# Performance work log

Hardware: AMD Instinct MI355X
Metric: run time of the kernel (lower is better)

## Reference

```python
import jax, jax.numpy as jnp
import numpy as np

NUM_EMBEDDINGS = 8192
EMBEDDING_DIM = 512
COMMITMENT_COST = 0.25
DECAY = 0.99
EPSILON = 1e-05


def _l2_normalize(x, axis=-1, eps=1e-12):
    # matches torch.nn.functional.normalize (p=2)
    n = jnp.sqrt(jnp.sum(x * x, axis=axis, keepdims=True))
    return x / jnp.maximum(n, eps)


def setup_inputs() -> dict:
    key = jax.random.key(0)
    k1, k2, k3 = jax.random.split(key, 3)
    inputs = jax.random.normal(k1, (8, 4096, EMBEDDING_DIM), dtype=jnp.float32)
    embedding = jax.random.normal(k2, (NUM_EMBEDDINGS, EMBEDDING_DIM), dtype=jnp.float32) * 0.01
    ema_cluster_size = jnp.ones((NUM_EMBEDDINGS,), dtype=jnp.float32)
    ema_w = jax.random.normal(k3, (NUM_EMBEDDINGS, EMBEDDING_DIM), dtype=jnp.float32) * 0.01
    return {"inputs": inputs, "embedding": embedding,
            "ema_cluster_size": ema_cluster_size, "ema_w": ema_w}


def reference(inputs, embedding, ema_cluster_size, ema_w):
    K, D = NUM_EMBEDDINGS, EMBEDDING_DIM
    flat = _l2_normalize(inputs.reshape(-1, D))           # [N, D]
    emb_n = _l2_normalize(embedding)                       # [K, D] (in-place normalize in torch)

    # cosine distance: 1 - flat @ emb^T  -> argmin
    distances = 1.0 - jnp.matmul(flat, emb_n.T)            # [N, K]
    idx = jnp.argmin(distances, axis=1)                    # [N]

    # one-hot @ codebook == gather
    quantized = jnp.take(emb_n, idx, axis=0).reshape(inputs.shape)

    # EMA codebook update (training branch), scatter-encode via segment_sum
    counts = jax.ops.segment_sum(jnp.ones_like(idx, dtype=flat.dtype), idx,
                                 num_segments=K)           # [K]
    new_cs = ema_cluster_size * DECAY + (1.0 - DECAY) * counts
    n = jnp.sum(new_cs)
    new_cs = (new_cs + EPSILON) / (n + K * EPSILON) * n
    dw = jax.ops.segment_sum(flat, idx, num_segments=K)    # [K, D] == one_hot^T @ flat
    new_ema_w = ema_w * DECAY + (1.0 - DECAY) * dw
    new_embedding = new_ema_w / jnp.clip(new_cs, EPSILON, None)[:, None]

    e_latent_loss = jnp.mean((jax.lax.stop_gradient(quantized) - inputs) ** 2)
    loss = COMMITMENT_COST * e_latent_loss

    quantized_st = inputs + jax.lax.stop_gradient(quantized - inputs)
    encoding_indices = idx.reshape(inputs.shape[:-1])
    return (quantized_st, loss, encoding_indices, new_cs, new_ema_w, new_embedding)
```

## Files before the change

### kernel.cpp

```cpp
#include <hip/hip_runtime.h>
#include <math.h>

#define NROWS 32768
#define DIM   512
#define KCODE 8192
#define DECAYF 0.99f
#define OMDF   0.01f
#define EPSF   1e-5f
#define COMMITF 0.25f
#define MARGIN 8e-4f

typedef _Float16 half8 __attribute__((ext_vector_type(8)));
typedef _Float16 half4v __attribute__((ext_vector_type(4)));
typedef _Float16 half2v __attribute__((ext_vector_type(2)));
typedef float floatx16 __attribute__((ext_vector_type(16)));


__device__ __forceinline__ float block_sum_256(float v) {
    __shared__ float sm[4];
    int lane = threadIdx.x & 63, wave = threadIdx.x >> 6;
    #pragma unroll
    for (int off = 32; off; off >>= 1) v += __shfl_down(v, off);
    if (lane == 0) sm[wave] = v;
    __syncthreads();
    if (threadIdx.x == 0) v = sm[0] + sm[1] + sm[2] + sm[3];
    return v;
}

__global__ void k_rownorm_inv(const float* __restrict__ x, float* __restrict__ inv) {
    int wave = threadIdx.x >> 6;
    int lane = threadIdx.x & 63;
    int row = blockIdx.x * 4 + wave;
    const float* p = x + (size_t)row * DIM;
    float4 f1 = *(const float4*)&p[lane * 4];
    float4 f2 = *(const float4*)&p[256 + lane * 4];
    float s = f1.x*f1.x + f1.y*f1.y + f1.z*f1.z + f1.w*f1.w
            + f2.x*f2.x + f2.y*f2.y + f2.z*f2.z + f2.w*f2.w;
    #pragma unroll
    for (int off = 32; off; off >>= 1) s += __shfl_down(s, off);
    if (lane == 0) inv[row] = 1.0f / fmaxf(sqrtf(s), 1e-12f);
}

__global__ void k_split(const float* __restrict__ src, const float* __restrict__ inv,
                        _Float16* __restrict__ hi, _Float16* __restrict__ lo) {
    const int i4 = (blockIdx.x * 256 + threadIdx.x) * 4;
    const float iv = inv[i4 >> 9];
    const float4 v = *(const float4*)&src[i4];
    float n0 = v.x * iv, n1 = v.y * iv, n2 = v.z * iv, n3 = v.w * iv;
    _Float16 h0 = (_Float16)n0, h1 = (_Float16)n1, h2 = (_Float16)n2, h3 = (_Float16)n3;
    half4v hv = {h0, h1, h2, h3};
    *(half4v*)&hi[i4] = hv;
    half4v lv = {(_Float16)((n0 - (float)h0) * 4096.f),
                 (_Float16)((n1 - (float)h1) * 4096.f),
                 (_Float16)((n2 - (float)h2) * 4096.f),
                 (_Float16)((n3 - (float)h3) * 4096.f)};
    *(half4v*)&lo[i4] = lv;
}

__device__ __forceinline__ void gld16(const _Float16* g, _Float16* l) {
    __builtin_amdgcn_global_load_lds(
        (const __attribute__((address_space(1))) void*)g,
        (__attribute__((address_space(3))) void*)l, 16, 0, 0);
}

__device__ __forceinline__ void top2_upd(float v, int i, float& v1, int& i1, float& v2) {
    if (v > v1) { v2 = v1; v1 = v; i1 = i; }
    else        { v2 = fmaxf(v2, v); }
}

__launch_bounds__(256, 2)
__global__ void k_hi(const _Float16* __restrict__ Xh, const _Float16* __restrict__ Eh,
                     float* __restrict__ sV1, float* __restrict__ sV2,
                     unsigned short* __restrict__ sI1) {
    __shared__ __align__(16) _Float16 lds[24576];
    __shared__ float mV[128][2], mV2[128][2];
    __shared__ int   mI[128][2];

    const int tid  = threadIdx.x;
    const int w    = tid >> 6;
    const int lane = tid & 63;
    const int wc = w & 1, wr = w >> 1;
    const int c = lane & 31, h = lane >> 5;
    const int rowBase = blockIdx.x * 128;
    const int split   = blockIdx.y;
    const int sr = lane >> 3;
    const int sg = (lane & 7) ^ (sr & 7);
    const int cx = c & 7;
    const int rowB = wr * 64 + c;

    float v1a = -1e30f, v2a = -1e30f, v1b = -1e30f, v2b = -1e30f;
    int i1a = 0, i1b = 0;

    for (int nt = 0; nt < 16; ++nt) {
        const int ntBase = split * 4096 + nt * 256;
        floatx16 acc[4][2];
        #pragma unroll
        for (int i = 0; i < 4; ++i)
            #pragma unroll
            for (int j = 0; j < 2; ++j)
                #pragma unroll
                for (int r = 0; r < 16; ++r) acc[i][j][r] = 0.f;

        for (int chunk = 0; chunk < 8; ++chunk) {
            const int kt = chunk * 64;
            #pragma unroll
            for (int j = 0; j < 12; ++j) {
                const int u0 = w * 96 + j * 8;
                const int u  = u0 + sr;
                if (u0 < 256) {
                    gld16(Eh + (size_t)(ntBase + u) * DIM + kt + sg * 8, &lds[u0 * 64]);
                } else {
                    gld16(Xh + (size_t)(rowBase + u - 256) * DIM + kt + sg * 8,
                          &lds[16384 + (u0 - 256) * 64]);
                }
            }
            __syncthreads();
            #pragma unroll
            for (int ks = 0; ks < 4; ++ks) {
                const int so = ((ks * 2 + h) ^ cx) * 8;
                half8 a0 = *(const half8*)&lds[(wc * 128 + 0  + c) * 64 + so];
                half8 a1 = *(const half8*)&lds[(wc * 128 + 32 + c) * 64 + so];
                half8 a2 = *(const half8*)&lds[(wc * 128 + 64 + c) * 64 + so];
                half8 a3 = *(const half8*)&lds[(wc * 128 + 96 + c) * 64 + so];
                half8 b0 = *(const half8*)&lds[16384 + (rowB) * 64 + so];
                half8 b1 = *(const half8*)&lds[16384 + (rowB + 32) * 64 + so];
                acc[0][0] = __builtin_amdgcn_mfma_f32_32x32x16_f16(a0, b0, acc[0][0], 0, 0, 0);
                acc[1][0] = __builtin_amdgcn_mfma_f32_32x32x16_f16(a1, b0, acc[1][0], 0, 0, 0);
                acc[2][0] = __builtin_amdgcn_mfma_f32_32x32x16_f16(a2, b0, acc[2][0], 0, 0, 0);
                acc[3][0] = __builtin_amdgcn_mfma_f32_32x32x16_f16(a3, b0, acc[3][0], 0, 0, 0);
                acc[0][1] = __builtin_amdgcn_mfma_f32_32x32x16_f16(a0, b1, acc[0][1], 0, 0, 0);
                acc[1][1] = __builtin_amdgcn_mfma_f32_32x32x16_f16(a1, b1, acc[1][1], 0, 0, 0);
                acc[2][1] = __builtin_amdgcn_mfma_f32_32x32x16_f16(a2, b1, acc[2][1], 0, 0, 0);
                acc[3][1] = __builtin_amdgcn_mfma_f32_32x32x16_f16(a3, b1, acc[3][1], 0, 0, 0);
            }
            __syncthreads();
        }
        #pragma unroll
        for (int r = 0; r < 16; ++r) {
            const int codeSub = (r & 3) + ((r >> 2) << 3) + (h << 2);
            #pragma unroll
            for (int i = 0; i < 4; ++i) {
                const int code = ntBase + wc * 128 + i * 32 + codeSub;
                top2_upd(acc[i][0][r], code, v1a, i1a, v2a);
                top2_upd(acc[i][1][r], code, v1b, i1b, v2b);
            }
        }
    }

    {
        float ov1 = __shfl_xor(v1a, 32); int oi1 = __shfl_xor(i1a, 32); float ov2 = __shfl_xor(v2a, 32);
        if (ov1 > v1a) { v2a = fmaxf(v1a, ov2); v1a = ov1; i1a = oi1; }
        else if (ov1 == v1a) { v2a = v1a; if (oi1 < i1a) i1a = oi1; }
        else { v2a = fmaxf(v2a, ov1); }
        ov1 = __shfl_xor(v1b, 32); oi1 = __shfl_xor(i1b, 32); ov2 = __shfl_xor(v2b, 32);
        if (ov1 > v1b) { v2b = fmaxf(v1b, ov2); v1b = ov1; i1b = oi1; }
        else if (ov1 == v1b) { v2b = v1b; if (oi1 < i1b) i1b = oi1; }
        else { v2b = fmaxf(v2b, ov1); }
    }
    if (h == 0) {
        mV[rowB][wc] = v1a; mV2[rowB][wc] = v2a; mI[rowB][wc] = i1a;
        mV[rowB + 32][wc] = v1b; mV2[rowB + 32][wc] = v2b; mI[rowB + 32][wc] = i1b;
    }
    __syncthreads();
    if (tid < 128) {
        float v1 = mV[tid][0], v2 = mV2[tid][0]; int i1 = mI[tid][0];
        float ov1 = mV[tid][1], ov2 = mV2[tid][1]; int oi1 = mI[tid][1];
        if (ov1 > v1) { v2 = fmaxf(v1, ov2); v1 = ov1; i1 = oi1; }
        else if (ov1 == v1) { v2 = v1; if (oi1 < i1) i1 = oi1; }
        else { v2 = fmaxf(v2, ov1); }
        const int n = rowBase + tid;
        sV1[split * NROWS + n] = v1;
        sV2[split * NROWS + n] = v2;
        sI1[split * NROWS + n] = (unsigned short)i1;
    }
}

__global__ void k_top2_merge(const float* __restrict__ sV1, const float* __restrict__ sV2,
                             const unsigned short* __restrict__ sI1,
                             float* __restrict__ outIdx, int* __restrict__ list,
                             int* __restrict__ flagCnt) {
    const int n = blockIdx.x * 256 + threadIdx.x;
    float a1 = sV1[n], a2 = sV2[n]; int ai = sI1[n];
    float b1 = sV1[NROWS + n], b2 = sV2[NROWS + n]; int bi = sI1[NROWS + n];
    float best, run; int bidx;
    if (b1 > a1) { best = b1; bidx = bi; run = fmaxf(a1, b2); }
    else         { best = a1; bidx = ai; run = fmaxf(a2, b1); }
    outIdx[n] = (float)bidx;
    if (best - run < MARGIN) {
        int p = atomicAdd(flagCnt, 1);
        list[p] = n;
    }
}

__device__ __forceinline__ unsigned long long encodeKey(float v, int idx) {
    unsigned u = __float_as_uint(v);
    u = (u & 0x80000000u) ? ~u : (u | 0x80000000u);
    return ((unsigned long long)u << 32) | (unsigned)(0xFFFFFFFFu - (unsigned)idx);
}

__launch_bounds__(256, 2)
__global__ void k_rescore(const _Float16* __restrict__ Xh, const _Float16* __restrict__ Xl,
                          const _Float16* __restrict__ Eh, const _Float16* __restrict__ El,
                          const int* __restrict__ list, const int* __restrict__ flagCnt,
                          unsigned long long* __restrict__ rkey) {
    const int cnt = *flagCnt;
    const int t = blockIdx.x & 255;
    const int s = blockIdx.x >> 8;
    if (t * 128 >= cnt) return;

    __shared__ __align__(16) _Float16 lds[32768];
    __shared__ float mV[128][2];
    __shared__ int   mI[128][2];

    const int tid  = threadIdx.x;
    const int w    = tid >> 6;
    const int lane = tid & 63;
    const int wc = w & 1, wr = w >> 1;
    const int c = lane & 31, h = lane >> 5;
    const int sr = lane >> 3;
    const int sg = (lane & 7) ^ (sr & 7);
    const int rowA = wc * 64 + c;
    const int rowB = wr * 64 + c;
    const int cx = c & 7;

    int rows_j[4];
    #pragma unroll
    for (int j = 0; j < 4; ++j) {
        const int slot = t * 128 + w * 32 + j * 8 + sr;
        rows_j[j] = (slot < cnt) ? list[slot] : 0;
    }

    float best0 = -1e30f, best1 = -1e30f;
    int bi0 = 0, bi1 = 0;
    const float SC = 1.0f / 4096.0f;

    for (int nt = 0; nt < 4; ++nt) {
        const int ntBase = s * 512 + nt * 128;

        floatx16 accH00, accH01, accH10, accH11, accC00, accC01, accC10, accC11;
        #pragma unroll
        for (int r = 0; r < 16; ++r) {
            accH00[r] = 0.f; accH01[r] = 0.f; accH10[r] = 0.f; accH11[r] = 0.f;
            accC00[r] = 0.f; accC01[r] = 0.f; accC10[r] = 0.f; accC11[r] = 0.f;
        }

        for (int chunk = 0; chunk < 8; ++chunk) {
            const int kt = chunk * 64;
            #pragma unroll
            for (int j = 0; j < 4; ++j) {
                const int rl = w * 32 + j * 8 + sr;
                const size_t gE = (size_t)(ntBase + rl) * DIM + kt + sg * 8;
                const size_t gX = (size_t)rows_j[j] * DIM + kt + sg * 8;
                _Float16* dBase = &lds[(w * 32 + j * 8) * 64];
                gld16(Eh + gE, dBase);
                gld16(El + gE, dBase + 8192);
                gld16(Xh + gX, dBase + 16384);
                gld16(Xl + gX, dBase + 24576);
            }
            __syncthreads();
            #pragma unroll
            for (int ks = 0; ks < 4; ++ks) {
                const int so = ((ks * 2 + h) ^ cx) * 8;
                const half8 ah0 = *(const half8*)&lds[rowA * 64 + so];
                const half8 ah1 = *(const half8*)&lds[(rowA + 32) * 64 + so];
                const half8 al0 = *(const half8*)&lds[8192 + rowA * 64 + so];
                const half8 al1 = *(const half8*)&lds[8192 + (rowA + 32) * 64 + so];
                const half8 bh0 = *(const half8*)&lds[16384 + rowB * 64 + so];
                const half8 bh1 = *(const half8*)&lds[16384 + (rowB + 32) * 64 + so];
                const half8 bl0 = *(const half8*)&lds[24576 + rowB * 64 + so];
                const half8 bl1 = *(const half8*)&lds[24576 + (rowB + 32) * 64 + so];

                accH00 = __builtin_amdgcn_mfma_f32_32x32x16_f16(ah0, bh0, accH00, 0, 0, 0);
                accC00 = __builtin_amdgcn_mfma_f32_32x32x16_f16(ah0, bl0, accC00, 0, 0, 0);
                accC00 = __builtin_amdgcn_mfma_f32_32x32x16_f16(al0, bh0, accC00, 0, 0, 0);

                accH01 = __builtin_amdgcn_mfma_f32_32x32x16_f16(ah0, bh1, accH01, 0, 0, 0);
                accC01 = __builtin_amdgcn_mfma_f32_32x32x16_f16(ah0, bl1, accC01, 0, 0, 0);
                accC01 = __builtin_amdgcn_mfma_f32_32x32x16_f16(al0, bh1, accC01, 0, 0, 0);

                accH10 = __builtin_amdgcn_mfma_f32_32x32x16_f16(ah1, bh0, accH10, 0, 0, 0);
                accC10 = __builtin_amdgcn_mfma_f32_32x32x16_f16(ah1, bl0, accC10, 0, 0, 0);
                accC10 = __builtin_amdgcn_mfma_f32_32x32x16_f16(al1, bh0, accC10, 0, 0, 0);

                accH11 = __builtin_amdgcn_mfma_f32_32x32x16_f16(ah1, bh1, accH11, 0, 0, 0);
                accC11 = __builtin_amdgcn_mfma_f32_32x32x16_f16(ah1, bl1, accC11, 0, 0, 0);
                accC11 = __builtin_amdgcn_mfma_f32_32x32x16_f16(al1, bh1, accC11, 0, 0, 0);
            }
            __syncthreads();
        }

        #pragma unroll
        for (int r = 0; r < 16; ++r) {
            const int codeSub = (r & 3) + ((r >> 2) << 3) + (h << 2);
            const int code0 = ntBase + wc * 64 + codeSub;
            const int code1 = code0 + 32;
            float v;
            v = fmaf(accC00[r], SC, accH00[r]);
            if (v > best0 || (v == best0 && code0 < bi0)) { best0 = v; bi0 = code0; }
            v = fmaf(accC10[r], SC, accH10[r]);
            if (v > best0 || (v == best0 && code1 < bi0)) { best0 = v; bi0 = code1; }
            v = fmaf(accC01[r], SC, accH01[r]);
            if (v > best1 || (v == best1 && code0 < bi1)) { best1 = v; bi1 = code0; }
            v = fmaf(accC11[r], SC, accH11[r]);
            if (v > best1 || (v == best1 && code1 < bi1)) { best1 = v; bi1 = code1; }
        }
    }

    {
        float ov = __shfl_xor(best0, 32); int oi = __shfl_xor(bi0, 32);
        if (ov > best0 || (ov == best0 && oi < bi0)) { best0 = ov; bi0 = oi; }
        ov = __shfl_xor(best1, 32); oi = __shfl_xor(bi1, 32);
        if (ov > best1 || (ov == best1 && oi < bi1)) { best1 = ov; bi1 = oi; }
    }
    if (h == 0) {
        mV[rowB][wc] = best0;      mI[rowB][wc] = bi0;
        mV[rowB + 32][wc] = best1; mI[rowB + 32][wc] = bi1;
    }
    __syncthreads();
    if (tid < 128) {
        const int slot = t * 128 + tid;
        if (slot < cnt) {
            float v0 = mV[tid][0]; int i0 = mI[tid][0];
            float v1 = mV[tid][1]; int i1 = mI[tid][1];
            float bv; int bidx;
            if (v1 > v0 || (v1 == v0 && i1 < i0)) { bv = v1; bidx = i1; }
            else                                  { bv = v0; bidx = i0; }
            atomicMax(&rkey[list[slot]], encodeKey(bv, bidx));
        }
    }
}

__global__ void k_rescore_merge(const unsigned long long* __restrict__ rkey,
                                const int* __restrict__ list, const int* __restrict__ flagCnt,
                                float* __restrict__ outIdx) {
    const int slot = blockIdx.x * 256 + threadIdx.x;
    if (slot < *flagCnt) {
        const int row = list[slot];
        const unsigned long long key = rkey[row];
        const int code = (int)(0xFFFFFFFFu - (unsigned)(key & 0xFFFFFFFFull));
        outIdx[row] = (float)code;
    }
}

__global__ void k_hist(const float* __restrict__ outIdx, int* __restrict__ cntI) {
    const int n = blockIdx.x * 256 + threadIdx.x;
    atomicAdd(&cntI[(int)outIdx[n]], 1);
}

__global__ void k_gather_loss(const float* __restrict__ X, const _Float16* __restrict__ Eh,
                              const _Float16* __restrict__ El, const float* __restrict__ outIdx,
                              float* __restrict__ qst, float* __restrict__ lossAcc) {
    const float SC = 1.0f / 4096.0f;
    float acc = 0.f;
    #pragma unroll
    for (int it = 0; it < 8; ++it) {
        const int e = (it * 2048 + blockIdx.x) * 256 + threadIdx.x;
        const int row = e >> 7;
        const int col = (e & 127) * 4;
        const int k = (int)outIdx[row];
        const float4 x = ((const float4*)X)[e];
        const half4v eh = *(const half4v*)&Eh[(size_t)k * DIM + col];
        const half4v el = *(const half4v*)&El[(size_t)k * DIM + col];
        const float q0 = (float)eh.x + (float)el.x * SC;
        const float q1 = (float)eh.y + (float)el.y * SC;
        const float q2 = (float)eh.z + (float)el.z * SC;
        const float q3 = (float)eh.w + (float)el.w * SC;
        const float d0 = q0 - x.x, d1 = q1 - x.y, d2 = q2 - x.z, d3 = q3 - x.w;
        float4 o; o.x = x.x + d0; o.y = x.y + d1; o.z = x.z + d2; o.w = x.w + d3;
        ((float4*)qst)[e] = o;
        acc += d0 * d0 + d1 * d1 + d2 * d2 + d3 * d3;
    }
    const float ls = block_sum_256(acc);
    if (threadIdx.x == 0) atomicAdd(lossAcc, ls);
}

__global__ void k_cs_pre(const float* __restrict__ emacs, const int* __restrict__ cntI,
                         float* __restrict__ pre, float* __restrict__ nsum) {
    const int k = blockIdx.x * 256 + threadIdx.x;
    float p = emacs[k] * DECAYF + OMDF * (float)cntI[k];
    pre[k] = p;
    float s = block_sum_256(p);
    if (threadIdx.x == 0) atomicAdd(nsum, s);
}

__global__ void k_cs_final(const float* __restrict__ pre, const float* __restrict__ nsum,
                           float* __restrict__ outCS, float* __restrict__ csfin,
                           const float* __restrict__ lossAcc, float* __restrict__ outLoss) {
    const int k = blockIdx.x * 256 + threadIdx.x;
    float n = *nsum;
    float c = (pre[k] + EPSF) / (n + (float)KCODE * EPSF) * n;
    outCS[k] = c;
    csfin[k] = c;
    if (k == 0) *outLoss = COMMITF * (*lossAcc) / (float)(NROWS * DIM);
}

__global__ void k_scan(const int* __restrict__ cntI, int* __restrict__ offs) {
    __shared__ int ps[1024];
    const int t = threadIdx.x;
    int loc[8], pref[8], s = 0;
    #pragma unroll
    for (int j = 0; j < 8; ++j) { loc[j] = cntI[t * 8 + j]; pref[j] = s; s += loc[j]; }
    ps[t] = s;
    __syncthreads();
    for (int d = 1; d < 1024; d <<= 1) {
        int x = (t >= d) ? ps[t - d] : 0;
        __syncthreads();
        ps[t] += x;
        __syncthreads();
    }
    const int base = ps[t] - s;
    #pragma unroll
    for (int j = 0; j < 8; ++j) offs[t * 8 + j] = base + pref[j];
}

__global__ void k_bin(const float* __restrict__ outIdx, const int* __restrict__ offs,
                      int* __restrict__ cursor, int* __restrict__ perm) {
    const int n = blockIdx.x * 256 + threadIdx.x;
    const int k = (int)outIdx[n];
    const int pos = offs[k] + atomicAdd(&cursor[k], 1);
    perm[pos] = n;
}

__global__ void k_dw_fused(const float* __restrict__ X, const float* __restrict__ inv_in,
                           const int* __restrict__ perm, const int* __restrict__ offs,
                           const int* __restrict__ cntI, const float* __restrict__ emaw,
                           const float* __restrict__ csfin,
                           float* __restrict__ outW, float* __restrict__ outE) {
    const int k = blockIdx.x;
    const int t = threadIdx.x;
    const int c = cntI[k];
    const int base = offs[k];
    float a0 = 0.f, a1 = 0.f;
    for (int i = 0; i < c; ++i) {
        const int row = perm[base + i];
        const float iv = inv_in[row];
        const float2 x = *(const float2*)&X[(size_t)row * DIM + t * 2];
        a0 = fmaf(x.x, iv, a0);
        a1 = fmaf(x.y, iv, a1);
    }
    const float2 w2 = *(const float2*)&emaw[(size_t)k * DIM + t * 2];
    const float w0 = w2.x * DECAYF + OMDF * a0;
    const float w1 = w2.y * DECAYF + OMDF * a1;
    float2 ow; ow.x = w0; ow.y = w1;
    *(float2*)&outW[(size_t)k * DIM + t * 2] = ow;
    const float cs = fmaxf(csfin[k], EPSF);
    float2 oe; oe.x = w0 / cs; oe.y = w1 / cs;
    *(float2*)&outE[(size_t)k * DIM + t * 2] = oe;
}

extern "C" void kernel_launch(void* const* d_in, const int* in_sizes, int n_in,
                              void* d_out, int out_size, void* d_ws, size_t ws_size,
                              hipStream_t stream) {
    const float* inputs    = (const float*)d_in[0];
    const float* embedding = (const float*)d_in[1];
    const float* emacs     = (const float*)d_in[2];
    const float* emaw      = (const float*)d_in[3];
    float* out = (float*)d_out;
    float* ws  = (float*)d_ws;

    float* inv_in  = ws;
    float* sV1     = ws + 32768;
    float* sV2     = ws + 98304;
    unsigned short* sI1 = (unsigned short*)(ws + 163840);
    int*   list    = (int*)(ws + 196608);
    int*   flagCnt = (int*)(ws + 229376);
    float* inv_emb = ws + 229440;
    _Float16* Xh   = (_Float16*)(ws + 229440);
    _Float16* Xl   = (_Float16*)(ws + 8618048);
    _Float16* Eh   = (_Float16*)(ws + 17006656);
    _Float16* El   = (_Float16*)(ws + 19103808);
    unsigned long long* rkey = (unsigned long long*)(ws + 32768);
    int*   cntI    = (int*)(ws + 98304);
    int*   cursor  = (int*)(ws + 106496);
    float* lossAcc = ws + 114688;
    float* nsum    = ws + 114689;
    float* pre     = ws + 114692;
    float* csfin   = ws + 122884;
    int*   offs    = (int*)(ws + 131076);
    int*   perm    = (int*)(ws + 139268);

    float* outQst  = out;
    float* outLoss = out + 16777216;
    float* outIdx  = out + 16777217;
    float* outCS   = out + 16809985;
    float* outW    = out + 16818177;
    float* outE    = out + 21012481;

    hipMemsetAsync(flagCnt, 0, sizeof(int), stream);
    k_rownorm_inv<<<NROWS / 4, 256, 0, stream>>>(inputs, inv_in);
    k_rownorm_inv<<<KCODE / 4, 256, 0, stream>>>(embedding, inv_emb);
    k_split<<<KCODE * DIM / 1024, 256, 0, stream>>>(embedding, inv_emb, Eh, El);
    k_split<<<NROWS * DIM / 1024, 256, 0, stream>>>(inputs, inv_in, Xh, Xl);
    k_hi<<<dim3(NROWS / 128, 2), 256, 0, stream>>>(Xh, Eh, sV1, sV2, sI1);
    k_top2_merge<<<NROWS / 256, 256, 0, stream>>>(sV1, sV2, sI1, outIdx, list, flagCnt);
    hipMemsetAsync(ws + 32768, 0, (size_t)81922 * sizeof(float), stream);
    k_rescore<<<4096, 256, 0, stream>>>(Xh, Xl, Eh, El, list, flagCnt, rkey);
    k_rescore_merge<<<NROWS / 256, 256, 0, stream>>>(rkey, list, flagCnt, outIdx);
    k_hist<<<NROWS / 256, 256, 0, stream>>>(outIdx, cntI);
    k_gather_loss<<<2048, 256, 0, stream>>>(inputs, Eh, El, outIdx, outQst, lossAcc);
    k_cs_pre<<<KCODE / 256, 256, 0, stream>>>(emacs, cntI, pre, nsum);
    k_cs_final<<<KCODE / 256, 256, 0, stream>>>(pre, nsum, outCS, csfin, lossAcc, outLoss);
    k_scan<<<1, 1024, 0, stream>>>(cntI, offs);
    k_bin<<<NROWS / 256, 256, 0, stream>>>(outIdx, offs, cursor, perm);
    k_dw_fused<<<KCODE, 256, 0, stream>>>(inputs, inv_in, perm, offs, cntI, emaw, csfin,
                                          outW, outE);
}
```

Before: 679.6 us.

## Triple-buffer LDS staging with async prefetch in distance GEMM kernel

Replaces the single-buffered, two-barrier-per-chunk K loop with a three-stage ring of 32-wide K slices. Global-to-LDS loads for step s+2 are issued while step s is computed, using an explicit vmcnt wait and one barrier per step. It also changes the LDS swizzle to fit the narrower rows and raises wave priority around the MFMA burst. The cost targeted is memory latency exposed between load and compute, in exchange for more LDS per block (about 72KB), which may limit occupancy, and more barriers per K element.

```diff
diff --git a/kernel.cpp b/kernel.cpp
--- a/kernel.cpp
+++ b/kernel.cpp
@@ -68,11 +68,28 @@
     else        { v2 = fmaxf(v2, v); }
 }
 
+__device__ __forceinline__ void stage_step(const _Float16* __restrict__ Xh,
+                                           const _Float16* __restrict__ Eh,
+                                           _Float16* dst, int split, int rowBase,
+                                           int ss, int w, int rg, int colOff) {
+    const int ntB = split * 4096 + (ss >> 4) * 256;
+    const int kts = (ss & 15) << 5;
+    #pragma unroll
+    for (int j = 0; j < 6; ++j) {
+        const int m = w * 6 + j;
+        const int r = m * 16 + rg;
+        const _Float16* src = (m < 16)
+            ? (Eh + (size_t)(ntB + r) * DIM + (kts + colOff))
+            : (Xh + (size_t)(rowBase + (r - 256)) * DIM + (kts + colOff));
+        gld16(src, dst + m * 512);
+    }
+}
+
 __launch_bounds__(256, 2)
 __global__ void k_hi(const _Float16* __restrict__ Xh, const _Float16* __restrict__ Eh,
                      float* __restrict__ sV1, float* __restrict__ sV2,
                      unsigned short* __restrict__ sI1) {
-    __shared__ __align__(16) _Float16 lds[24576];
+    __shared__ __align__(16) _Float16 lds[3 * 12288];
     __shared__ float mV[128][2], mV2[128][2];
     __shared__ int   mI[128][2];
 
@@ -83,13 +100,20 @@
     const int c = lane & 31, h = lane >> 5;
     const int rowBase = blockIdx.x * 128;
     const int split   = blockIdx.y;
-    const int sr = lane >> 3;
-    const int sg = (lane & 7) ^ (sr & 7);
-    const int cx = c & 7;
+
+    const int rg   = lane >> 2;
+    const int slot = lane & 3;
+    const int colOff = (slot ^ ((rg ^ (rg >> 2)) & 3)) * 8;
+
+    const int Pc = (c ^ (c >> 2)) & 3;
     const int rowB = wr * 64 + c;
 
     float v1a = -1e30f, v2a = -1e30f, v1b = -1e30f, v2b = -1e30f;
     int i1a = 0, i1b = 0;
+
+    stage_step(Xh, Eh, &lds[0],     split, rowBase, 0, w, rg, colOff);
+    stage_step(Xh, Eh, &lds[12288], split, rowBase, 1, w, rg, colOff);
+    int br = 0, bs = 2;
 
     for (int nt = 0; nt < 16; ++nt) {
         const int ntBase = split * 4096 + nt * 256;
@@ -101,29 +125,26 @@
                 #pragma unroll
                 for (int r = 0; r < 16; ++r) acc[i][j][r] = 0.f;
 
-        for (int chunk = 0; chunk < 8; ++chunk) {
-            const int kt = chunk * 64;
+        for (int kt16 = 0; kt16 < 16; ++kt16) {
+            const int s = nt * 16 + kt16;
+            asm volatile("s_waitcnt vmcnt(6)" ::: "memory");
+            __builtin_amdgcn_sched_barrier(0);
+            __builtin_amdgcn_s_barrier();
+            __builtin_amdgcn_sched_barrier(0);
+            stage_step(Xh, Eh, &lds[bs * 12288], split, rowBase,
+                       (s + 2) & 255, w, rg, colOff);
+            __builtin_amdgcn_sched_barrier(0);
+            const _Float16* B = &lds[br * 12288];
             #pragma unroll
-            for (int j = 0; j < 12; ++j) {
-                const int u0 = w * 96 + j * 8;
-                const int u  = u0 + sr;
-                if (u0 < 256) {
-                    gld16(Eh + (size_t)(ntBase + u) * DIM + kt + sg * 8, &lds[u0 * 64]);
-                } else {
-                    gld16(Xh + (size_t)(rowBase + u - 256) * DIM + kt + sg * 8,
-                          &lds[16384 + (u0 - 256) * 64]);
-                }
-            }
-            __syncthreads();
-            #pragma unroll
-            for (int ks = 0; ks < 4; ++ks) {
-                const int so = ((ks * 2 + h) ^ cx) * 8;
-                half8 a0 = *(const half8*)&lds[(wc * 128 + 0  + c) * 64 + so];
-                half8 a1 = *(const half8*)&lds[(wc * 128 + 32 + c) * 64 + so];
-                half8 a2 = *(const half8*)&lds[(wc * 128 + 64 + c) * 64 + so];
-                half8 a3 = *(const half8*)&lds[(wc * 128 + 96 + c) * 64 + so];
-                half8 b0 = *(const half8*)&lds[16384 + (rowB) * 64 + so];
-                half8 b1 = *(const half8*)&lds[16384 + (rowB + 32) * 64 + so];
+            for (int ks = 0; ks < 2; ++ks) {
+                const int so = (((ks << 1) + h) ^ Pc) << 3;
+                half8 a0 = *(const half8*)&B[(wc * 128 +  0 + c) * 32 + so];
+                half8 a1 = *(const half8*)&B[(wc * 128 + 32 + c) * 32 + so];
+                half8 a2 = *(const half8*)&B[(wc * 128 + 64 + c) * 32 + so];
+                half8 a3 = *(const half8*)&B[(wc * 128 + 96 + c) * 32 + so];
+                half8 b0 = *(const half8*)&B[8192 + (rowB) * 32 + so];
+                half8 b1 = *(const half8*)&B[8192 + (rowB + 32) * 32 + so];
+                __builtin_amdgcn_s_setprio(1);
                 acc[0][0] = __builtin_amdgcn_mfma_f32_32x32x16_f16(a0, b0, acc[0][0], 0, 0, 0);
                 acc[1][0] = __builtin_amdgcn_mfma_f32_32x32x16_f16(a1, b0, acc[1][0], 0, 0, 0);
                 acc[2][0] = __builtin_amdgcn_mfma_f32_32x32x16_f16(a2, b0, acc[2][0], 0, 0, 0);
@@ -132,8 +153,10 @@
                 acc[1][1] = __builtin_amdgcn_mfma_f32_32x32x16_f16(a1, b1, acc[1][1], 0, 0, 0);
                 acc[2][1] = __builtin_amdgcn_mfma_f32_32x32x16_f16(a2, b1, acc[2][1], 0, 0, 0);
                 acc[3][1] = __builtin_amdgcn_mfma_f32_32x32x16_f16(a3, b1, acc[3][1], 0, 0, 0);
+                __builtin_amdgcn_s_setprio(0);
             }
-            __syncthreads();
+            br = (br == 2) ? 0 : br + 1;
+            bs = (bs == 2) ? 0 : bs + 1;
         }
         #pragma unroll
         for (int r = 0; r < 16; ++r) {
```

Result: slower. 728.3 us (+7.2%).
